# Kernel tuning notes

Hardware: AMD Instinct MI355X
Metric: run time of the kernel (lower is better)

Reference implementation:

```python
import jax, jax.numpy as jnp
import numpy as np

N = 100000      # nodes
E = 1600000     # edges (avg degree 16)
G = 1000        # graphs in batch
F_IN = 128      # num_features
C = 10          # num_classes
EPS = 1e-5


def setup_inputs() -> dict:
    key = jax.random.key(0)
    ks = jax.random.split(key, 12)
    w = lambda k, shape: jax.random.normal(k, shape, jnp.float32) * 0.05
    return {
        'x': jax.random.normal(ks[0], (N, F_IN), jnp.float32),
        'edge_index': jax.random.randint(ks[1], (2, E), 0, N, jnp.int32),
        'edge_weights': jax.random.randint(ks[2], (E,), 0, 2, jnp.int32),
        'batch': jnp.sort(jax.random.randint(ks[3], (N,), 0, G, jnp.int32)),
        'num_graphs': G,
        # initial MLP: Linear(128,32)+BN+ReLU, Linear(32,32)+BN+ReLU
        'W1': w(ks[4], (F_IN, 32)), 'b1': jnp.zeros(32), 'g1': jnp.ones(32), 'bt1': jnp.zeros(32),
        'W2': w(ks[5], (32, 32)), 'b2': jnp.zeros(32), 'g2': jnp.ones(32), 'bt2': jnp.zeros(32),
        'Wl0': w(ks[6], (32, C)), 'bl0': jnp.zeros(C),   # initial_linear
        'Wg1': w(ks[7], (32, 64)), 'bg1': jnp.zeros(64),  # GCNConv 1
        'Wl1': w(ks[8], (64, C)), 'bl1': jnp.zeros(C),
        'Wg2': w(ks[9], (64, 64)), 'bg2': jnp.zeros(64),  # GCNConv 2
        'Wl2': w(ks[10], (64, C)), 'bl2': jnp.zeros(C),
    }


def _bn(h, gamma, beta):
    # BatchNorm1d in training mode: biased batch statistics over nodes
    mu = h.mean(0)
    var = ((h - mu) ** 2).mean(0)
    return gamma * (h - mu) * jax.lax.rsqrt(var + EPS) + beta


def _gcn(h_in, row, col, w, W, b):
    # PyG GCNConv with self-loops: D^{-1/2}(A+I)D^{-1/2} X W + b,
    # edges with mask weight 0 contribute nothing (incl. to degree).
    n = h_in.shape[0]
    h = h_in @ W
    deg = jax.ops.segment_sum(w, col, num_segments=n) + 1.0  # +1 self-loop
    dinv = jax.lax.rsqrt(deg)
    norm = w * dinv[row] * dinv[col]                  # [E]
    agg = jax.ops.segment_sum(h[row] * norm[:, None], col, num_segments=n)
    agg = agg + h * (dinv * dinv)[:, None]            # self-loop term
    return agg + b


def _pool_max(h, batch, num_graphs):
    # torch_scatter scatter_max readout; empty segments -> 0
    p = jax.ops.segment_max(h, batch, num_segments=num_graphs)
    return jnp.where(jnp.isfinite(p), p, 0.0)


def reference(x, edge_index, edge_weights, batch, num_graphs,
              W1, b1, g1, bt1, W2, b2, g2, bt2, Wl0, bl0,
              Wg1, bg1, Wl1, bl1, Wg2, bg2, Wl2, bl2):
    row, col = edge_index[0], edge_index[1]
    w = (edge_weights == 1).astype(x.dtype)  # boolean edge mask as 0/1 weight
    # initial MLP (dropout treated as identity for deterministic reference)
    h = jax.nn.relu(_bn(x @ W1 + b1, g1, bt1))
    h = jax.nn.relu(_bn(h @ W2 + b2, g2, bt2))
    out = _pool_max(h @ Wl0 + bl0, batch, num_graphs)
    # layer 1
    h = _gcn(h, row, col, w, Wg1, bg1)
    out = out + _pool_max(h, batch, num_graphs) @ Wl1 + bl1
    # layer 2
    h = _gcn(h, row, col, w, Wg2, bg2)
    out = out + _pool_max(h, batch, num_graphs) @ Wl2 + bl2
    return out
```

## Files before the change

kernel.cpp:

```cpp
#include <hip/hip_runtime.h>

#define NN 100000
#define EE 1600000
#define GG 1000
#define BN_EPS 1e-5f
#define NB1 391

__device__ __forceinline__ unsigned encf(float f){
  unsigned u = __float_as_uint(f);
  return (u & 0x80000000u) ? ~u : (u | 0x80000000u);
}
__device__ __forceinline__ float dec0(unsigned e){
  unsigned u = (e & 0x80000000u) ? (e & 0x7fffffffu) : ~e;
  float f = __uint_as_float(u);
  return isfinite(f) ? f : 0.0f;
}
__device__ __forceinline__ unsigned short f2bf(float f){
  unsigned u = __float_as_uint(f);
  u += 0x7FFFu + ((u >> 16) & 1u);
  return (unsigned short)(u >> 16);
}
__device__ __forceinline__ float bf2f(unsigned short s){
  return __uint_as_float(((unsigned)s) << 16);
}

__global__ void k_count(const int* __restrict__ ei, const int* __restrict__ ew,
                        int* __restrict__ cnt){
  int e = blockIdx.x*256 + threadIdx.x;
  if (e < EE && ew[e] == 1) atomicAdd(&cnt[ei[EE + e]], 1);
}

__global__ __launch_bounds__(256) void k_scan1(const int* __restrict__ cnt,
    int* __restrict__ loc, int* __restrict__ bsum){
  __shared__ int sm[256];
  const int i = blockIdx.x*256 + threadIdx.x;
  const int v = (i < NN) ? cnt[i] : 0;
  sm[threadIdx.x] = v;
  __syncthreads();
  for (int off = 1; off < 256; off <<= 1){
    int t = (threadIdx.x >= off) ? sm[threadIdx.x - off] : 0;
    __syncthreads();
    sm[threadIdx.x] += t;
    __syncthreads();
  }
  if (i < NN) loc[i] = sm[threadIdx.x] - v;
  if (threadIdx.x == 255) bsum[blockIdx.x] = sm[255];
}

__global__ __launch_bounds__(512) void k_scan2(const int* __restrict__ bsum,
    int* __restrict__ boff){
  __shared__ int sm[512];
  const int t = threadIdx.x;
  const int v = (t < NB1) ? bsum[t] : 0;
  sm[t] = v;
  __syncthreads();
  for (int off = 1; off < 512; off <<= 1){
    int x = (t >= off) ? sm[t - off] : 0;
    __syncthreads();
    sm[t] += x;
    __syncthreads();
  }
  if (t <= NB1) boff[t] = sm[t] - v;
}

__global__ void k_fin(const int* __restrict__ cnt, const int* __restrict__ loc,
                      const int* __restrict__ boff, float* __restrict__ dinv,
                      int* __restrict__ rowstart, int* __restrict__ fill){
  const int i = blockIdx.x*256 + threadIdx.x;
  if (i < NN){
    int rs = loc[i] + boff[i >> 8];
    rowstart[i] = rs; fill[i] = rs;
    dinv[i] = rsqrtf((float)cnt[i] + 1.0f);
  } else if (i == NN){
    rowstart[NN] = boff[NB1];
  }
}

__global__ void k_scatter(const int* __restrict__ ei, const int* __restrict__ ew,
                          int* __restrict__ fill, int* __restrict__ csr){
  int e = blockIdx.x*256 + threadIdx.x;
  if (e < EE && ew[e] == 1){
    int c = ei[EE + e];
    int pos = atomicAdd(&fill[c], 1);
    csr[pos] = ei[e];
  }
}

__global__ __launch_bounds__(256) void k_gemm1(const float* __restrict__ x,
    const float* __restrict__ W1, const float* __restrict__ b1,
    float* __restrict__ Y1, float* __restrict__ stats){
  __shared__ float xs[32*132];
  __shared__ float Ws[128*32];
  __shared__ float red[64];
  const int tid = threadIdx.x;
  for (int j = tid; j < 1024; j += 256) ((float4*)Ws)[j] = ((const float4*)W1)[j];
  const int r = tid >> 3, cg = tid & 7;
  const float4 bv = ((const float4*)b1)[cg];
  float s0=0,s1=0,s2=0,s3=0,q0=0,q1=0,q2=0,q3=0;
  for (int tile = blockIdx.x; tile < 3125; tile += gridDim.x){
    __syncthreads();
    for (int j = tid; j < 1024; j += 256){
      int rr = j >> 5, kk = j & 31;
      *(float4*)&xs[rr*132 + kk*4] = ((const float4*)x)[(size_t)tile*1024 + j];
    }
    __syncthreads();
    float a0=bv.x, a1=bv.y, a2=bv.z, a3=bv.w;
    const float* xr = &xs[r*132];
    const float* wc = &Ws[cg*4];
    #pragma unroll 8
    for (int k = 0; k < 128; k++){
      float xv = xr[k];
      float4 w = *(const float4*)&wc[k*32];
      a0 += xv*w.x; a1 += xv*w.y; a2 += xv*w.z; a3 += xv*w.w;
    }
    float4 o; o.x=a0; o.y=a1; o.z=a2; o.w=a3;
    ((float4*)Y1)[(size_t)(tile*32 + r)*8 + cg] = o;
    s0+=a0; s1+=a1; s2+=a2; s3+=a3;
    q0+=a0*a0; q1+=a1*a1; q2+=a2*a2; q3+=a3*a3;
  }
  __syncthreads();
  if (tid < 64) red[tid] = 0.f;
  __syncthreads();
  atomicAdd(&red[cg*4+0], s0); atomicAdd(&red[cg*4+1], s1);
  atomicAdd(&red[cg*4+2], s2); atomicAdd(&red[cg*4+3], s3);
  atomicAdd(&red[32+cg*4+0], q0); atomicAdd(&red[32+cg*4+1], q1);
  atomicAdd(&red[32+cg*4+2], q2); atomicAdd(&red[32+cg*4+3], q3);
  __syncthreads();
  if (tid < 64) atomicAdd(&stats[tid], red[tid]);
}

__global__ __launch_bounds__(256) void k_mlp2(const float* __restrict__ Y1,
    const float* __restrict__ W2, const float* __restrict__ b2,
    const float* __restrict__ g1, const float* __restrict__ bt1,
    float* __restrict__ stats, float* __restrict__ Y2){
  __shared__ float hs[32*36];
  __shared__ float Ws[32*32];
  __shared__ float red[64];
  __shared__ float scs[32], shs[32];
  const int tid = threadIdx.x;
  ((float4*)Ws)[tid] = ((const float4*)W2)[tid];
  if (tid < 32){
    float mean = stats[tid] * (1.0f/NN);
    float var  = stats[32 + tid] * (1.0f/NN) - mean*mean;
    float s = g1[tid] * rsqrtf(fmaxf(var, 0.0f) + BN_EPS);
    scs[tid] = s; shs[tid] = bt1[tid] - mean*s;
  }
  __syncthreads();
  const int r = tid >> 3, cg = tid & 7;
  const float4 bv = ((const float4*)b2)[cg];
  const float4 sc = *(const float4*)&scs[cg*4];
  const float4 sh = *(const float4*)&shs[cg*4];
  float s0=0,s1=0,s2=0,s3=0,q0=0,q1=0,q2=0,q3=0;
  for (int tile = blockIdx.x; tile < 3125; tile += gridDim.x){
    __syncthreads();
    {
      float4 v = ((const float4*)Y1)[(size_t)tile*256 + tid];
      v.x = fmaxf(fmaf(v.x, sc.x, sh.x), 0.f);
      v.y = fmaxf(fmaf(v.y, sc.y, sh.y), 0.f);
      v.z = fmaxf(fmaf(v.z, sc.z, sh.z), 0.f);
      v.w = fmaxf(fmaf(v.w, sc.w, sh.w), 0.f);
      *(float4*)&hs[r*36 + cg*4] = v;
    }
    __syncthreads();
    float a0=bv.x, a1=bv.y, a2=bv.z, a3=bv.w;
    const float* hr = &hs[r*36];
    const float* wc = &Ws[cg*4];
    #pragma unroll
    for (int k = 0; k < 32; k++){
      float h = hr[k];
      float4 w = *(const float4*)&wc[k*32];
      a0 += h*w.x; a1 += h*w.y; a2 += h*w.z; a3 += h*w.w;
    }
    float4 o; o.x=a0; o.y=a1; o.z=a2; o.w=a3;
    ((float4*)Y2)[(size_t)(tile*32 + r)*8 + cg] = o;
    s0+=a0; s1+=a1; s2+=a2; s3+=a3;
    q0+=a0*a0; q1+=a1*a1; q2+=a2*a2; q3+=a3*a3;
  }
  __syncthreads();
  if (tid < 64) red[tid] = 0.f;
  __syncthreads();
  atomicAdd(&red[cg*4+0], s0); atomicAdd(&red[cg*4+1], s1);
  atomicAdd(&red[cg*4+2], s2); atomicAdd(&red[cg*4+3], s3);
  atomicAdd(&red[32+cg*4+0], q0); atomicAdd(&red[32+cg*4+1], q1);
  atomicAdd(&red[32+cg*4+2], q2); atomicAdd(&red[32+cg*4+3], q3);
  __syncthreads();
  if (tid < 64) atomicAdd(&stats[128 + tid], red[tid]);
}

__global__ __launch_bounds__(256) void k_layer0(const float* __restrict__ Y2,
    const float* __restrict__ stats, const float* __restrict__ g2,
    const float* __restrict__ bt2, const float* __restrict__ Wg1,
    const float* __restrict__ Wl0, const float* __restrict__ bl0,
    const float* __restrict__ dinv, const int* __restrict__ batch,
    unsigned short* __restrict__ Hs1, unsigned* __restrict__ Pool0){
  __shared__ float hs[32*36];
  __shared__ float Wg[32*64];
  __shared__ float Wl[320];
  __shared__ float bl[10];
  __shared__ float scs[32], shs[32];
  const int tid = threadIdx.x;
  ((float4*)Wg)[tid]       = ((const float4*)Wg1)[tid];
  ((float4*)Wg)[tid + 256] = ((const float4*)Wg1)[tid + 256];
  for (int j = tid; j < 320; j += 256) Wl[j] = Wl0[j];
  if (tid < 10)  bl[tid] = bl0[tid];
  if (tid < 32){
    float mean = stats[128 + tid] * (1.0f/NN);
    float var  = stats[160 + tid] * (1.0f/NN) - mean*mean;
    float s = g2[tid] * rsqrtf(fmaxf(var, 0.0f) + BN_EPS);
    scs[tid] = s; shs[tid] = bt2[tid] - mean*s;
  }
  __syncthreads();
  {
    const int rr = tid >> 3, kk = tid & 7;
    const float4 sc = *(const float4*)&scs[kk*4];
    const float4 sh = *(const float4*)&shs[kk*4];
    float4 v = ((const float4*)Y2)[(size_t)blockIdx.x*256 + tid];
    v.x = fmaxf(fmaf(v.x, sc.x, sh.x), 0.f);
    v.y = fmaxf(fmaf(v.y, sc.y, sh.y), 0.f);
    v.z = fmaxf(fmaf(v.z, sc.z, sh.z), 0.f);
    v.w = fmaxf(fmaf(v.w, sc.w, sh.w), 0.f);
    *(float4*)&hs[rr*36 + kk*4] = v;
  }
  __syncthreads();
  const int w = tid >> 6, f = tid & 63;
  for (int i = 0; i < 8; i++){
    const int r = w*8 + i;
    const int row = blockIdx.x*32 + r;
    const float* hr = &hs[r*36];
    float acc = 0.f;
    #pragma unroll
    for (int k = 0; k < 32; k++) acc += hr[k]*Wg[k*64 + f];
    Hs1[(size_t)row*64 + f] = f2bf(acc * dinv[row]);
    if (f < 10){
      float p = bl[f];
      #pragma unroll
      for (int k = 0; k < 32; k++) p += hr[k]*Wl[k*10 + f];
      atomicMax(&Pool0[batch[row]*10 + f], encf(p));
    }
  }
}

__device__ __forceinline__ float gather_sum(const unsigned short* __restrict__ Hs,
    const int* __restrict__ csr, int s, int e, int f){
  float acc = 0.f;
  int j = s;
  for (; j + 7 < e; j += 8){
    const int r0 = csr[j],   r1 = csr[j+1], r2 = csr[j+2], r3 = csr[j+3];
    const int r4 = csr[j+4], r5 = csr[j+5], r6 = csr[j+6], r7 = csr[j+7];
    float t0 = bf2f(Hs[(size_t)r0*64 + f]);
    float t1 = bf2f(Hs[(size_t)r1*64 + f]);
    float t2 = bf2f(Hs[(size_t)r2*64 + f]);
    float t3 = bf2f(Hs[(size_t)r3*64 + f]);
    float t4 = bf2f(Hs[(size_t)r4*64 + f]);
    float t5 = bf2f(Hs[(size_t)r5*64 + f]);
    float t6 = bf2f(Hs[(size_t)r6*64 + f]);
    float t7 = bf2f(Hs[(size_t)r7*64 + f]);
    acc += ((t0 + t1) + (t2 + t3)) + ((t4 + t5) + (t6 + t7));
  }
  for (; j + 3 < e; j += 4){
    const int r0 = csr[j], r1 = csr[j+1], r2 = csr[j+2], r3 = csr[j+3];
    float t0 = bf2f(Hs[(size_t)r0*64 + f]);
    float t1 = bf2f(Hs[(size_t)r1*64 + f]);
    float t2 = bf2f(Hs[(size_t)r2*64 + f]);
    float t3 = bf2f(Hs[(size_t)r3*64 + f]);
    acc += (t0 + t1) + (t2 + t3);
  }
  for (; j < e; j++) acc += bf2f(Hs[(size_t)csr[j]*64 + f]);
  return acc;
}

__device__ __forceinline__ void pool_epilogue(float h, int w, int f, int c,
    const int* __restrict__ batch, unsigned* __restrict__ Pool,
    float (*sm)[64], int* sb){
  sm[w][f] = h;
  if (f == 0) sb[w] = batch[c];
  __syncthreads();
  if (w == 0){
    const int b0 = sb[0], b1 = sb[1], b2 = sb[2], b3 = sb[3];
    if (b0 == b3){
      float m = fmaxf(fmaxf(sm[0][f], sm[1][f]), fmaxf(sm[2][f], sm[3][f]));
      atomicMax(&Pool[b0*64 + f], encf(m));
    } else {
      atomicMax(&Pool[b0*64 + f], encf(sm[0][f]));
      atomicMax(&Pool[b1*64 + f], encf(sm[1][f]));
      atomicMax(&Pool[b2*64 + f], encf(sm[2][f]));
      atomicMax(&Pool[b3*64 + f], encf(sm[3][f]));
    }
  }
}

__global__ __launch_bounds__(256) void k_agg1(const unsigned short* __restrict__ Hs,
    const float* __restrict__ dinv, const int* __restrict__ rowstart,
    const int* __restrict__ csr, const float* __restrict__ bias,
    const int* __restrict__ batch, unsigned short* __restrict__ H2b,
    unsigned* __restrict__ Pool){
  __shared__ float sm[4][64];
  __shared__ int sb[4];
  const int w = threadIdx.x >> 6, f = threadIdx.x & 63;
  const int c = blockIdx.x*4 + w;
  const int s = rowstart[c], e = rowstart[c+1];
  float acc = gather_sum(Hs, csr, s, e, f);
  const float dc = dinv[c];
  const float h = fmaf(acc + bf2f(Hs[(size_t)c*64 + f]), dc, bias[f]);
  H2b[(size_t)c*64 + f] = f2bf(h);
  pool_epilogue(h, w, f, c, batch, Pool, sm, sb);
}

__global__ __launch_bounds__(256) void k_agg2(const unsigned short* __restrict__ Hs,
    const float* __restrict__ dinv, const int* __restrict__ rowstart,
    const int* __restrict__ csr, const float* __restrict__ bias,
    const int* __restrict__ batch, unsigned* __restrict__ Pool){
  __shared__ float sm[4][64];
  __shared__ int sb[4];
  const int w = threadIdx.x >> 6, f = threadIdx.x & 63;
  const int c = blockIdx.x*4 + w;
  const int s = rowstart[c], e = rowstart[c+1];
  float acc = gather_sum(Hs, csr, s, e, f);
  const float dc = dinv[c];
  const float h = fmaf(acc + bf2f(Hs[(size_t)c*64 + f]), dc, bias[f]);
  pool_epilogue(h, w, f, c, batch, Pool, sm, sb);
}

__global__ __launch_bounds__(256) void k_layer1(const unsigned short* __restrict__ H2b,
    const float* __restrict__ Wg2, const float* __restrict__ dinv,
    unsigned short* __restrict__ Hs2){
  __shared__ float as[32*68];
  __shared__ float Wg[64*64];
  const int tid = threadIdx.x;
  #pragma unroll
  for (int j = 0; j < 4; j++) ((float4*)Wg)[tid + j*256] = ((const float4*)Wg2)[tid + j*256];
  {
    const int rr = tid >> 3, kk = tid & 7;
    ushort4 v0 = ((const ushort4*)H2b)[(size_t)blockIdx.x*512 + tid*2];
    ushort4 v1 = ((const ushort4*)H2b)[(size_t)blockIdx.x*512 + tid*2 + 1];
    float* dst = &as[rr*68 + kk*8];
    dst[0]=bf2f(v0.x); dst[1]=bf2f(v0.y); dst[2]=bf2f(v0.z); dst[3]=bf2f(v0.w);
    dst[4]=bf2f(v1.x); dst[5]=bf2f(v1.y); dst[6]=bf2f(v1.z); dst[7]=bf2f(v1.w);
  }
  __syncthreads();
  const int w = tid >> 6, f = tid & 63;
  for (int i = 0; i < 8; i++){
    const int r = w*8 + i;
    const int row = blockIdx.x*32 + r;
    const float* ar = &as[r*68];
    float acc = 0.f;
    #pragma unroll
    for (int k = 0; k < 64; k++) acc += ar[k]*Wg[k*64 + f];
    Hs2[(size_t)row*64 + f] = f2bf(acc * dinv[row]);
  }
}

__global__ __launch_bounds__(256) void k_final(const unsigned* __restrict__ P0,
    const unsigned* __restrict__ P1, const unsigned* __restrict__ P2,
    const float* __restrict__ Wl1, const float* __restrict__ bl1,
    const float* __restrict__ Wl2, const float* __restrict__ bl2,
    float* __restrict__ out){
  const int t = blockIdx.x*256 + threadIdx.x;
  const int g = t >> 4, c = t & 15;
  if (g >= GG || c >= 10) return;
  float acc = dec0(P0[g*10 + c]) + bl1[c] + bl2[c];
  for (int f = 0; f < 64; f++){
    acc += dec0(P1[g*64 + f]) * Wl1[f*10 + c];
    acc += dec0(P2[g*64 + f]) * Wl2[f*10 + c];
  }
  out[g*10 + c] = acc;
}

extern "C" void kernel_launch(void* const* d_in, const int* in_sizes, int n_in,
                              void* d_out, int out_size, void* d_ws, size_t ws_size,
                              hipStream_t stream){
  const float* x   = (const float*)d_in[0];
  const int*   ei  = (const int*)d_in[1];
  const int*   ew  = (const int*)d_in[2];
  const int*   bat = (const int*)d_in[3];
  const float* W1  = (const float*)d_in[5],  *b1  = (const float*)d_in[6];
  const float* g1  = (const float*)d_in[7],  *bt1 = (const float*)d_in[8];
  const float* W2  = (const float*)d_in[9],  *b2  = (const float*)d_in[10];
  const float* g2  = (const float*)d_in[11], *bt2 = (const float*)d_in[12];
  const float* Wl0 = (const float*)d_in[13], *bl0 = (const float*)d_in[14];
  const float* Wg1 = (const float*)d_in[15], *bg1 = (const float*)d_in[16];
  const float* Wl1 = (const float*)d_in[17], *bl1 = (const float*)d_in[18];
  const float* Wg2 = (const float*)d_in[19], *bg2 = (const float*)d_in[20];
  const float* Wl2 = (const float*)d_in[21], *bl2 = (const float*)d_in[22];

  float* ws = (float*)d_ws;
  const size_t oCnt   = 0;
  const size_t oStats = NN;
  const size_t oP0    = oStats + 256;
  const size_t oP1    = oP0 + (size_t)GG*10;
  const size_t oP2    = oP1 + (size_t)GG*64;
  const size_t oZEnd  = oP2 + (size_t)GG*64;
  const size_t oDinv  = oZEnd;
  const size_t oLoc   = oDinv + NN;
  const size_t oBsum  = oLoc + NN;
  const size_t oBoff  = oBsum + 512;
  const size_t oRS    = oBoff + 512;
  const size_t oFill  = oRS + NN + 8;
  const size_t oCsr   = oFill + NN;
  const size_t oA     = oCsr + EE;
  const size_t oHs1   = oA + (size_t)NN*64;

  int*   cnt   = (int*)(ws + oCnt);
  float* stats = ws + oStats;
  unsigned* P0 = (unsigned*)(ws + oP0);
  unsigned* P1 = (unsigned*)(ws + oP1);
  unsigned* P2 = (unsigned*)(ws + oP2);
  float* dinv  = ws + oDinv;
  int*   loc   = (int*)(ws + oLoc);
  int*   bsum  = (int*)(ws + oBsum);
  int*   boff  = (int*)(ws + oBoff);
  int*   rs    = (int*)(ws + oRS);
  int*   fill  = (int*)(ws + oFill);
  int*   csr   = (int*)(ws + oCsr);
  float* Y1    = ws + oA;
  float* Y2    = ws + oA + (size_t)NN*32;
  unsigned short* H2b = (unsigned short*)(ws + oA);
  unsigned short* Hs1 = (unsigned short*)(ws + oHs1);
  unsigned short* Hs2 = (unsigned short*)(ws + oA + (size_t)NN*32);

  (void)hipMemsetAsync(d_ws, 0, oZEnd*sizeof(float), stream);

  k_count  <<<EE/256, 256, 0, stream>>>(ei, ew, cnt);
  k_scan1  <<<NB1, 256, 0, stream>>>(cnt, loc, bsum);
  k_scan2  <<<1, 512, 0, stream>>>(bsum, boff);
  k_fin    <<<NB1, 256, 0, stream>>>(cnt, loc, boff, dinv, rs, fill);
  k_scatter<<<EE/256, 256, 0, stream>>>(ei, ew, fill, csr);

  k_gemm1<<<1536, 256, 0, stream>>>(x, W1, b1, Y1, stats);
  k_mlp2 <<<1536, 256, 0, stream>>>(Y1, W2, b2, g1, bt1, stats, Y2);
  k_layer0<<<3125, 256, 0, stream>>>(Y2, stats, g2, bt2, Wg1, Wl0, bl0, dinv, bat, Hs1, P0);
  k_agg1 <<<NN/4, 256, 0, stream>>>(Hs1, dinv, rs, csr, bg1, bat, H2b, P1);
  k_layer1<<<3125, 256, 0, stream>>>(H2b, Wg2, dinv, Hs2);
  k_agg2 <<<NN/4, 256, 0, stream>>>(Hs2, dinv, rs, csr, bg2, bat, P2);
  k_final<<<(GG*16 + 255)/256, 256, 0, stream>>>(P0, P1, P2, Wl1, bl1, Wl2, bl2, (float*)d_out);
}
```

Baseline: 336.8 us.

## Store MLP intermediates in bf16 and replace three-kernel scan with atomic block allocation

Result: slower. 354.8 us (+5.4%).

```diff
diff --git a/kernel.cpp b/kernel.cpp
--- a/kernel.cpp
+++ b/kernel.cpp
@@ -30,9 +30,11 @@
   if (e < EE && ew[e] == 1) atomicAdd(&cnt[ei[EE + e]], 1);
 }
 
-__global__ __launch_bounds__(256) void k_scan1(const int* __restrict__ cnt,
-    int* __restrict__ loc, int* __restrict__ bsum){
+__global__ __launch_bounds__(256) void k_alloc(const int* __restrict__ cnt,
+    int* __restrict__ ctr, float* __restrict__ dinv,
+    int* __restrict__ rowstart, int* __restrict__ fill){
   __shared__ int sm[256];
+  __shared__ int base;
   const int i = blockIdx.x*256 + threadIdx.x;
   const int v = (i < NN) ? cnt[i] : 0;
   sm[threadIdx.x] = v;
@@ -43,36 +45,12 @@
     sm[threadIdx.x] += t;
     __syncthreads();
   }
-  if (i < NN) loc[i] = sm[threadIdx.x] - v;
-  if (threadIdx.x == 255) bsum[blockIdx.x] = sm[255];
-}
-
-__global__ __launch_bounds__(512) void k_scan2(const int* __restrict__ bsum,
-    int* __restrict__ boff){
-  __shared__ int sm[512];
-  const int t = threadIdx.x;
-  const int v = (t < NB1) ? bsum[t] : 0;
-  sm[t] = v;
-  __syncthreads();
-  for (int off = 1; off < 512; off <<= 1){
-    int x = (t >= off) ? sm[t - off] : 0;
-    __syncthreads();
-    sm[t] += x;
-    __syncthreads();
-  }
-  if (t <= NB1) boff[t] = sm[t] - v;
-}
-
-__global__ void k_fin(const int* __restrict__ cnt, const int* __restrict__ loc,
-                      const int* __restrict__ boff, float* __restrict__ dinv,
-                      int* __restrict__ rowstart, int* __restrict__ fill){
-  const int i = blockIdx.x*256 + threadIdx.x;
+  if (threadIdx.x == 255) base = atomicAdd(ctr, sm[255]);
+  __syncthreads();
   if (i < NN){
-    int rs = loc[i] + boff[i >> 8];
+    int rs = base + sm[threadIdx.x] - v;
     rowstart[i] = rs; fill[i] = rs;
-    dinv[i] = rsqrtf((float)cnt[i] + 1.0f);
-  } else if (i == NN){
-    rowstart[NN] = boff[NB1];
+    dinv[i] = rsqrtf((float)v + 1.0f);
   }
 }
 
@@ -88,7 +66,7 @@
 
 __global__ __launch_bounds__(256) void k_gemm1(const float* __restrict__ x,
     const float* __restrict__ W1, const float* __restrict__ b1,
-    float* __restrict__ Y1, float* __restrict__ stats){
+    unsigned short* __restrict__ Y1b, float* __restrict__ stats){
   __shared__ float xs[32*132];
   __shared__ float Ws[128*32];
   __shared__ float red[64];
@@ -113,8 +91,8 @@
       float4 w = *(const float4*)&wc[k*32];
       a0 += xv*w.x; a1 += xv*w.y; a2 += xv*w.z; a3 += xv*w.w;
     }
-    float4 o; o.x=a0; o.y=a1; o.z=a2; o.w=a3;
-    ((float4*)Y1)[(size_t)(tile*32 + r)*8 + cg] = o;
+    ushort4 o; o.x=f2bf(a0); o.y=f2bf(a1); o.z=f2bf(a2); o.w=f2bf(a3);
+    ((ushort4*)Y1b)[(size_t)(tile*32 + r)*8 + cg] = o;
     s0+=a0; s1+=a1; s2+=a2; s3+=a3;
     q0+=a0*a0; q1+=a1*a1; q2+=a2*a2; q3+=a3*a3;
   }
@@ -129,10 +107,10 @@
   if (tid < 64) atomicAdd(&stats[tid], red[tid]);
 }
 
-__global__ __launch_bounds__(256) void k_mlp2(const float* __restrict__ Y1,
+__global__ __launch_bounds__(256) void k_mlp2(const unsigned short* __restrict__ Y1b,
     const float* __restrict__ W2, const float* __restrict__ b2,
     const float* __restrict__ g1, const float* __restrict__ bt1,
-    float* __restrict__ stats, float* __restrict__ Y2){
+    float* __restrict__ stats, unsigned short* __restrict__ Y2b){
   __shared__ float hs[32*36];
   __shared__ float Ws[32*32];
   __shared__ float red[64];
@@ -154,11 +132,12 @@
   for (int tile = blockIdx.x; tile < 3125; tile += gridDim.x){
     __syncthreads();
     {
-      float4 v = ((const float4*)Y1)[(size_t)tile*256 + tid];
-      v.x = fmaxf(fmaf(v.x, sc.x, sh.x), 0.f);
-      v.y = fmaxf(fmaf(v.y, sc.y, sh.y), 0.f);
-      v.z = fmaxf(fmaf(v.z, sc.z, sh.z), 0.f);
-      v.w = fmaxf(fmaf(v.w, sc.w, sh.w), 0.f);
+      ushort4 u = ((const ushort4*)Y1b)[(size_t)tile*256 + tid];
+      float4 v;
+      v.x = fmaxf(fmaf(bf2f(u.x), sc.x, sh.x), 0.f);
+      v.y = fmaxf(fmaf(bf2f(u.y), sc.y, sh.y), 0.f);
+      v.z = fmaxf(fmaf(bf2f(u.z), sc.z, sh.z), 0.f);
+      v.w = fmaxf(fmaf(bf2f(u.w), sc.w, sh.w), 0.f);
       *(float4*)&hs[r*36 + cg*4] = v;
     }
     __syncthreads();
@@ -171,8 +150,8 @@
       float4 w = *(const float4*)&wc[k*32];
       a0 += h*w.x; a1 += h*w.y; a2 += h*w.z; a3 += h*w.w;
     }
-    float4 o; o.x=a0; o.y=a1; o.z=a2; o.w=a3;
-    ((float4*)Y2)[(size_t)(tile*32 + r)*8 + cg] = o;
+    ushort4 o; o.x=f2bf(a0); o.y=f2bf(a1); o.z=f2bf(a2); o.w=f2bf(a3);
+    ((ushort4*)Y2b)[(size_t)(tile*32 + r)*8 + cg] = o;
     s0+=a0; s1+=a1; s2+=a2; s3+=a3;
     q0+=a0*a0; q1+=a1*a1; q2+=a2*a2; q3+=a3*a3;
   }
@@ -187,7 +166,7 @@
   if (tid < 64) atomicAdd(&stats[128 + tid], red[tid]);
 }
 
-__global__ __launch_bounds__(256) void k_layer0(const float* __restrict__ Y2,
+__global__ __launch_bounds__(256) void k_layer0(const unsigned short* __restrict__ Y2b,
     const float* __restrict__ stats, const float* __restrict__ g2,
     const float* __restrict__ bt2, const float* __restrict__ Wg1,
     const float* __restrict__ Wl0, const float* __restrict__ bl0,
@@ -214,11 +193,12 @@
     const int rr = tid >> 3, kk = tid & 7;
     const float4 sc = *(const float4*)&scs[kk*4];
     const float4 sh = *(const float4*)&shs[kk*4];
-    float4 v = ((const float4*)Y2)[(size_t)blockIdx.x*256 + tid];
-    v.x = fmaxf(fmaf(v.x, sc.x, sh.x), 0.f);
-    v.y = fmaxf(fmaf(v.y, sc.y, sh.y), 0.f);
-    v.z = fmaxf(fmaf(v.z, sc.z, sh.z), 0.f);
-    v.w = fmaxf(fmaf(v.w, sc.w, sh.w), 0.f);
+    ushort4 u = ((const ushort4*)Y2b)[(size_t)blockIdx.x*256 + tid];
+    float4 v;
+    v.x = fmaxf(fmaf(bf2f(u.x), sc.x, sh.x), 0.f);
+    v.y = fmaxf(fmaf(bf2f(u.y), sc.y, sh.y), 0.f);
+    v.z = fmaxf(fmaf(bf2f(u.z), sc.z, sh.z), 0.f);
+    v.w = fmaxf(fmaf(bf2f(u.w), sc.w, sh.w), 0.f);
     *(float4*)&hs[rr*36 + kk*4] = v;
   }
   __syncthreads();
@@ -291,30 +271,31 @@
 
 __global__ __launch_bounds__(256) void k_agg1(const unsigned short* __restrict__ Hs,
     const float* __restrict__ dinv, const int* __restrict__ rowstart,
-    const int* __restrict__ csr, const float* __restrict__ bias,
-    const int* __restrict__ batch, unsigned short* __restrict__ H2b,
+    const int* __restrict__ cnt, const int* __restrict__ csr,
+    const float* __restrict__ bias, const int* __restrict__ batch,
+    unsigned short* __restrict__ H2b, unsigned* __restrict__ Pool){
+  __shared__ float sm[4][64];
+  __shared__ int sb[4];
+  const int w = threadIdx.x >> 6, f = threadIdx.x & 63;
+  const int c = blockIdx.x*4 + w;
+  const int s = rowstart[c], e = s + cnt[c];
+  float acc = gather_sum(Hs, csr, s, e, f);
+  const float dc = dinv[c];
+  const float h = fmaf(acc + bf2f(Hs[(size_t)c*64 + f]), dc, bias[f]);
+  H2b[(size_t)c*64 + f] = f2bf(h);
+  pool_epilogue(h, w, f, c, batch, Pool, sm, sb);
+}
+
+__global__ __launch_bounds__(256) void k_agg2(const unsigned short* __restrict__ Hs,
+    const float* __restrict__ dinv, const int* __restrict__ rowstart,
+    const int* __restrict__ cnt, const int* __restrict__ csr,
+    const float* __restrict__ bias, const int* __restrict__ batch,
     unsigned* __restrict__ Pool){
   __shared__ float sm[4][64];
   __shared__ int sb[4];
   const int w = threadIdx.x >> 6, f = threadIdx.x & 63;
   const int c = blockIdx.x*4 + w;
-  const int s = rowstart[c], e = rowstart[c+1];
-  float acc = gather_sum(Hs, csr, s, e, f);
-  const float dc = dinv[c];
-  const float h = fmaf(acc + bf2f(Hs[(size_t)c*64 + f]), dc, bias[f]);
-  H2b[(size_t)c*64 + f] = f2bf(h);
-  pool_epilogue(h, w, f, c, batch, Pool, sm, sb);
-}
-
-__global__ __launch_bounds__(256) void k_agg2(const unsigned short* __restrict__ Hs,
-    const float* __restrict__ dinv, const int* __restrict__ rowstart,
-    const int* __restrict__ csr, const float* __restrict__ bias,
-    const int* __restrict__ batch, unsigned* __restrict__ Pool){
-  __shared__ float sm[4][64];
-  __shared__ int sb[4];
-  const int w = threadIdx.x >> 6, f = threadIdx.x & 63;
-  const int c = blockIdx.x*4 + w;
-  const int s = rowstart[c], e = rowstart[c+1];
+  const int s = rowstart[c], e = s + cnt[c];
   float acc = gather_sum(Hs, csr, s, e, f);
   const float dc = dinv[c];
   const float h = fmaf(acc + bf2f(Hs[(size_t)c*64 + f]), dc, bias[f]);
@@ -385,52 +366,48 @@
 
   float* ws = (float*)d_ws;
   const size_t oCnt   = 0;
-  const size_t oStats = NN;
+  const size_t oCtr   = NN;
+  const size_t oStats = NN + 8;
   const size_t oP0    = oStats + 256;
   const size_t oP1    = oP0 + (size_t)GG*10;
   const size_t oP2    = oP1 + (size_t)GG*64;
   const size_t oZEnd  = oP2 + (size_t)GG*64;
   const size_t oDinv  = oZEnd;
-  const size_t oLoc   = oDinv + NN;
-  const size_t oBsum  = oLoc + NN;
-  const size_t oBoff  = oBsum + 512;
-  const size_t oRS    = oBoff + 512;
-  const size_t oFill  = oRS + NN + 8;
+  const size_t oRS    = oDinv + NN;
+  const size_t oFill  = oRS + NN;
   const size_t oCsr   = oFill + NN;
-  const size_t oA     = oCsr + EE;
-  const size_t oHs1   = oA + (size_t)NN*64;
+  const size_t oR1    = oCsr + EE;
+  const size_t oR2    = oR1 + (size_t)NN*16;
+  const size_t oR3    = oR2 + (size_t)NN*16;
+  const size_t oR4    = oR3 + (size_t)NN*32;
 
   int*   cnt   = (int*)(ws + oCnt);
+  int*   ctr   = (int*)(ws + oCtr);
   float* stats = ws + oStats;
   unsigned* P0 = (unsigned*)(ws + oP0);
   unsigned* P1 = (unsigned*)(ws + oP1);
   unsigned* P2 = (unsigned*)(ws + oP2);
   float* dinv  = ws + oDinv;
-  int*   loc   = (int*)(ws + oLoc);
-  int*   bsum  = (int*)(ws + oBsum);
-  int*   boff  = (int*)(ws + oBoff);
   int*   rs    = (int*)(ws + oRS);
   int*   fill  = (int*)(ws + oFill);
   int*   csr   = (int*)(ws + oCsr);
-  float* Y1    = ws + oA;
-  float* Y2    = ws + oA + (size_t)NN*32;
-  unsigned short* H2b = (unsigned short*)(ws + oA);
-  unsigned short* Hs1 = (unsigned short*)(ws + oHs1);
-  unsigned short* Hs2 = (unsigned short*)(ws + oA + (size_t)NN*32);
+  unsigned short* Y1b = (unsigned short*)(ws + oR1);
+  unsigned short* Y2b = (unsigned short*)(ws + oR2);
+  unsigned short* Hs1 = (unsigned short*)(ws + oR3);
+  unsigned short* Hs2 = (unsigned short*)(ws + oR3);
+  unsigned short* H2b = (unsigned short*)(ws + oR4);
 
   (void)hipMemsetAsync(d_ws, 0, oZEnd*sizeof(float), stream);
 
   k_count  <<<EE/256, 256, 0, stream>>>(ei, ew, cnt);
-  k_scan1  <<<NB1, 256, 0, stream>>>(cnt, loc, bsum);
-  k_scan2  <<<1, 512, 0, stream>>>(bsum, boff);
-  k_fin    <<<NB1, 256, 0, stream>>>(cnt, loc, boff, dinv, rs, fill);
+  k_alloc  <<<NB1, 256, 0, stream>>>(cnt, ctr, dinv, rs, fill);
   k_scatter<<<EE/256, 256, 0, stream>>>(ei, ew, fill, csr);
 
-  k_gemm1<<<1536, 256, 0, stream>>>(x, W1, b1, Y1, stats);
-  k_mlp2 <<<1536, 256, 0, stream>>>(Y1, W2, b2, g1, bt1, stats, Y2);
-  k_layer0<<<3125, 256, 0, stream>>>(Y2, stats, g2, bt2, Wg1, Wl0, bl0, dinv, bat, Hs1, P0);
-  k_agg1 <<<NN/4, 256, 0, stream>>>(Hs1, dinv, rs, csr, bg1, bat, H2b, P1);
+  k_gemm1<<<1536, 256, 0, stream>>>(x, W1, b1, Y1b, stats);
+  k_mlp2 <<<1536, 256, 0, stream>>>(Y1b, W2, b2, g1, bt1, stats, Y2b);
+  k_layer0<<<3125, 256, 0, stream>>>(Y2b, stats, g2, bt2, Wg1, Wl0, bl0, dinv, bat, Hs1, P0);
+  k_agg1 <<<NN/4, 256, 0, stream>>>(Hs1, dinv, rs, cnt, csr, bg1, bat, H2b, P1);
   k_layer1<<<3125, 256, 0, stream>>>(H2b, Wg2, dinv, Hs2);
-  k_agg2 <<<NN/4, 256, 0, stream>>>(Hs2, dinv, rs, csr, bg2, bat, P2);
+  k_agg2 <<<NN/4, 256, 0, stream>>>(Hs2, dinv, rs, cnt, csr, bg2, bat, P2);
   k_final<<<(GG*16 + 255)/256, 256, 0, stream>>>(P0, P1, P2, Wl1, bl1, Wl2, bl2, (float*)d_out);
 }
```
